# Optimization experiments

Hardware: AMD Instinct MI355X
Metric: run time of the kernel (lower is better)

The kernel has to match this reference:

```python
import jax, jax.numpy as jnp
import numpy as np

B, W, L = 32768, 5, 20            # batch, words per example, max chars per word
WV, CV = 50000, 100               # word vocab, char vocab
CE, OC, K = 32, 30, 3             # char embed dim, conv out channels (=window_size), kernel
WE, HID, TAGS = 50, 100, 36       # word embed dim, fc1 hidden, output tags


def setup_inputs() -> dict:
    key = jax.random.key(0)
    ks = jax.random.split(key, 8)
    inp = jax.random.randint(ks[0], (B, W, 1 + L), 0, 100, dtype=jnp.int32)
    embedding_matrix = jax.random.normal(ks[1], (WV, WE), jnp.float32).at[0].set(0.0)  # padding_idx=0, frozen
    char_emb = jax.random.normal(ks[2], (CV, CE), jnp.float32).at[0].set(0.0)          # padding_idx=0
    conv_w = jax.random.normal(ks[3], (OC, CE, K), jnp.float32) * 0.1
    conv_b = jnp.zeros((OC,), jnp.float32)
    fc1_w = jax.random.normal(ks[4], (HID, (WE + OC) * W), jnp.float32) * 0.05
    fc1_b = jnp.zeros((HID,), jnp.float32)
    out_w = jax.random.normal(ks[5], (TAGS, HID), jnp.float32) * 0.1
    out_b = jnp.zeros((TAGS,), jnp.float32)
    return dict(input=inp, embedding_matrix=embedding_matrix, char_emb=char_emb,
                conv_w=conv_w, conv_b=conv_b, fc1_w=fc1_w, fc1_b=fc1_b,
                out_w=out_w, out_b=out_b)


def reference(input, embedding_matrix, char_emb, conv_w, conv_b, fc1_w, fc1_b, out_w, out_b):
    b = input.shape[0]
    word_ids = input[:, :, 0]                 # [B, W]
    char_ids = input[:, :, 1:]                # [B, W, L]
    we = embedding_matrix[word_ids]           # [B, W, 50]
    ce = char_emb[char_ids]                   # [B, W, L, CE]
    # conv1d over char axis, batched over all B*W words at once
    x = ce.reshape(b * W, L, CE).transpose(0, 2, 1)        # [B*W, CE, L]
    conv = jax.lax.conv_general_dilated(
        x, conv_w, window_strides=(1,), padding='VALID',
        dimension_numbers=('NCH', 'OIH', 'NCH')) + conv_b[None, :, None]  # [B*W, OC, L-2]
    pooled = conv.max(axis=2).reshape(b, W, OC)            # max pool over time
    feats = jnp.concatenate([we, pooled], axis=-1).reshape(b, -1)  # [B, (50+OC)*W]
    h = jnp.tanh(feats @ fc1_w.T + fc1_b)     # dropout is a no-op at inference
    return h @ out_w.T + out_b                # [B, 36]
```

## Files before the change

### kernel.cpp

```cpp
#include <hip/hip_runtime.h>

#define B_TOT 32768
#define OC 30
#define HID 100
#define TAGS 36

#define WS_TH  0
#define WS_FC1 6000
#define WS_OUT 29296
#define WS_F   40960

typedef __attribute__((ext_vector_type(8))) _Float16 half8;
typedef __attribute__((ext_vector_type(2))) _Float16 h2v;
typedef __attribute__((ext_vector_type(4))) float f32x4;

__device__ inline half8 ash8(uint4 u) {
    union { uint4 a; half8 b; } v; v.a = u; return v.b;
}
__device__ inline unsigned int h2u(h2v h) {
    union { h2v a; unsigned int b; } v; v.a = h; return v.b;
}
__device__ inline h2v u2h(unsigned int u) {
    union { unsigned int a; h2v b; } v; v.a = u; return v.b;
}
__device__ inline unsigned int pk_f16(float a, float b) {
    h2v h; h.x = (_Float16)a; h.y = (_Float16)b; return h2u(h);
}

__global__ void prep(const float* __restrict__ conv_w,
                     const float* __restrict__ char_emb,
                     const float* __restrict__ fc1_w,
                     const float* __restrict__ out_w,
                     unsigned int* __restrict__ ws) {
    int idx = blockIdx.x * 256 + threadIdx.x;
    if (idx < 6000) {
        int rd = idx % 20, row = idx / 20;
        int c = row % 100, k = row / 100;
        float v[2];
        #pragma unroll
        for (int e = 0; e < 2; ++e) {
            int oc = rd * 2 + e;
            float s = 0.f;
            if (oc < OC) {
                for (int ce = 0; ce < 32; ++ce)
                    s += char_emb[c * 32 + ce] * conv_w[(oc * 32 + ce) * 3 + k];
            }
            v[e] = s;
        }
        ws[WS_TH + idx] = pk_f16(v[0], v[1]);
    } else if (idx < 6000 + 23296) {
        int t = idx - 6000;
        int dw = t & 3, lane = (t >> 2) & 63, chunk = t >> 8;
        int ks = chunk % 13, nt = chunk / 13;
        int j = nt * 16 + (lane & 15);
        int k = ks * 32 + (lane >> 4) * 8 + dw * 2;
        float a = (j < HID && k     < 400) ? fc1_w[j * 400 + k]     : 0.f;
        float b = (j < HID && k + 1 < 400) ? fc1_w[j * 400 + k + 1] : 0.f;
        ws[WS_FC1 + t] = pk_f16(a, b);
    } else if (idx < 29296 + 3072) {
        int t = idx - 29296;
        int dw = t & 3, lane = (t >> 2) & 63, chunk = t >> 8;
        int ks = chunk % 4, nt = chunk / 4;
        int j = nt * 16 + (lane & 15);
        int k = ks * 32 + (lane >> 4) * 8 + dw * 2;
        float a = (j < TAGS && k     < HID) ? out_w[j * 100 + k]     : 0.f;
        float b = (j < TAGS && k + 1 < HID) ? out_w[j * 100 + k + 1] : 0.f;
        ws[WS_OUT + t] = pk_f16(a, b);
    }
}

__global__ __launch_bounds__(256)
void feat(const int*   __restrict__ input,
          const float* __restrict__ emb,
          const float* __restrict__ conv_b,
          unsigned int* __restrict__ ws)
{
    __shared__ unsigned int Ths[6000];

    const int tid   = threadIdx.x;
    const int item0 = blockIdx.x * 16;
    unsigned int* Fg = ws + WS_F;

    for (int idx = tid; idx < 6000; idx += 256) Ths[idx] = ws[WS_TH + idx];
    __syncthreads();

    if (tid < 128) Fg[(item0 + (tid >> 3)) * 208 + 200 + (tid & 7)] = 0;

    for (int idx = tid; idx < 2000; idx += 256) {
        int ph = idx % 25;
        int w  = (idx / 25) % 5;
        int i  = idx / 125;
        int wid = input[(item0 + i) * 105 + w * 21];
        float2 e = *(const float2*)&emb[wid * 50 + ph * 2];
        Fg[(item0 + i) * 208 + w * 40 + ph] = pk_f16(e.x, e.y);
    }

    {
        const int q4  = tid & 3;
        const int oc0 = q4 * 8;
        h2v bias[4];
        #pragma unroll
        for (int d = 0; d < 4; ++d) {
            int a = oc0 + 2 * d, b = a + 1;
            bias[d].x = (_Float16)(a < OC ? conv_b[a] : 0.f);
            bias[d].y = (_Float16)(b < OC ? conv_b[b] : 0.f);
        }
        for (int task = tid >> 2; task < 80; task += 64) {
            int i = task / 5, w = task % 5;
            const int* cp = &input[(item0 + i) * 105 + w * 21 + 1];
            int c[20];
            #pragma unroll
            for (int p = 0; p < 20; ++p) c[p] = cp[p];
            h2v m[4];
            #pragma unroll
            for (int d = 0; d < 4; ++d) { m[d].x = (_Float16)(-30000.f); m[d].y = (_Float16)(-30000.f); }
            #pragma unroll 6
            for (int p = 0; p < 18; ++p) {
                uint4 ra = *(const uint4*)&Ths[c[p    ] * 20        + q4 * 4];
                uint4 rb = *(const uint4*)&Ths[c[p + 1] * 20 + 2000 + q4 * 4];
                uint4 rc = *(const uint4*)&Ths[c[p + 2] * 20 + 4000 + q4 * 4];
                unsigned int* pa = (unsigned int*)&ra;
                unsigned int* pb = (unsigned int*)&rb;
                unsigned int* pc = (unsigned int*)&rc;
                #pragma unroll
                for (int d = 0; d < 4; ++d) {
                    h2v s = u2h(pa[d]) + u2h(pb[d]) + u2h(pc[d]);
                    m[d] = __builtin_elementwise_max(m[d], s);
                }
            }
            int base = (item0 + i) * 208 + w * 40 + 25 + q4 * 4;
            Fg[base]     = h2u(m[0] + bias[0]);
            Fg[base + 1] = h2u(m[1] + bias[1]);
            Fg[base + 2] = h2u(m[2] + bias[2]);
            if (q4 < 3) Fg[base + 3] = h2u(m[3] + bias[3]);
        }
    }
}

__global__ __launch_bounds__(256)
void gemm(const float* __restrict__ fc1_b,
          const float* __restrict__ out_b,
          const unsigned int* __restrict__ ws,
          float*       __restrict__ out)
{
    __shared__ unsigned int Hh[4][16 * 68];

    const int tid  = threadIdx.x;
    const int wv   = tid >> 6;
    const int lane = tid & 63;
    const int ln15 = lane & 15;
    const int quad = lane >> 4;
    const int item0 = blockIdx.x * 64 + wv * 16;
    unsigned int* Hw = &Hh[wv][0];
    const unsigned int* Fg = ws + WS_F;

    f32x4 acc[7];
    #pragma unroll
    for (int t = 0; t < 7; ++t) acc[t] = f32x4{0, 0, 0, 0};
    {
        const uint4* wp = (const uint4*)(ws + WS_FC1);
        const unsigned int* arow = Fg + (item0 + ln15) * 208 + quad * 4;
        for (int ks = 0; ks < 13; ++ks) {
            half8 a = ash8(*(const uint4*)(arow + ks * 16));
            #pragma unroll
            for (int t = 0; t < 7; ++t) {
                uint4 bv = wp[(t * 13 + ks) * 64 + lane];
                acc[t] = __builtin_amdgcn_mfma_f32_16x16x32_f16(a, ash8(bv), acc[t], 0, 0, 0);
            }
        }
    }

    {
        for (int t2 = lane; t2 < 224; t2 += 64) {
            int i = t2 / 14, d = t2 % 14;
            Hw[i * 68 + 50 + d] = 0;
        }
        unsigned short* Hs = (unsigned short*)Hw;
        #pragma unroll
        for (int t = 0; t < 7; ++t) {
            int j = t * 16 + ln15;
            if (j < HID) {
                float bj = fc1_b[j];
                #pragma unroll
                for (int r = 0; r < 4; ++r) {
                    int it = quad * 4 + r;
                    float hv = tanhf(acc[t][r] + bj);
                    _Float16 h = (_Float16)hv;
                    Hs[it * 136 + j] = *reinterpret_cast<unsigned short*>(&h);
                }
            }
        }
    }

    {
        f32x4 oacc[3];
        #pragma unroll
        for (int t = 0; t < 3; ++t) oacc[t] = f32x4{0, 0, 0, 0};
        const uint4* wpo = (const uint4*)(ws + WS_OUT);
        const int aoff = ln15 * 68 + quad * 4;
        #pragma unroll
        for (int ks = 0; ks < 4; ++ks) {
            half8 a = ash8(*(const uint4*)&Hw[aoff + ks * 16]);
            #pragma unroll
            for (int t = 0; t < 3; ++t) {
                uint4 bv = wpo[(t * 4 + ks) * 64 + lane];
                oacc[t] = __builtin_amdgcn_mfma_f32_16x16x32_f16(a, ash8(bv), oacc[t], 0, 0, 0);
            }
        }
        #pragma unroll
        for (int t = 0; t < 3; ++t) {
            int o = t * 16 + ln15;
            if (o < TAGS) {
                float bo = out_b[o];
                #pragma unroll
                for (int r = 0; r < 4; ++r) {
                    int it = item0 + quad * 4 + r;
                    out[it * TAGS + o] = oacc[t][r] + bo;
                }
            }
        }
    }
}

extern "C" void kernel_launch(void* const* d_in, const int* in_sizes, int n_in,
                              void* d_out, int out_size, void* d_ws, size_t ws_size,
                              hipStream_t stream) {
    const int*   input  = (const int*)  d_in[0];
    const float* emb    = (const float*)d_in[1];
    const float* char_e = (const float*)d_in[2];
    const float* conv_w = (const float*)d_in[3];
    const float* conv_b = (const float*)d_in[4];
    const float* fc1_w  = (const float*)d_in[5];
    const float* fc1_b  = (const float*)d_in[6];
    const float* out_w  = (const float*)d_in[7];
    const float* out_b  = (const float*)d_in[8];
    unsigned int* ws = (unsigned int*)d_ws;

    prep<<<127, 256, 0, stream>>>(conv_w, char_e, fc1_w, out_w, ws);
    feat<<<B_TOT / 16, 256, 0, stream>>>(input, emb, conv_b, ws);
    gemm<<<B_TOT / 64, 256, 0, stream>>>(fc1_b, out_b, ws, (float*)d_out);
}
```

Measured before the change: 127.5 us.

## Fuse feature extraction and MLP into one kernel with LDS-resident features

Merges the feat and gemm kernels so each wave builds its 16 items' feature rows in shared memory and runs the fc1/out MFMA GEMMs directly from LDS. This removes the global round trip of the fp16 feature buffer and one kernel launch. It also relays out the conv lookup table so each quarter-lane group reads a contiguous slice, and replaces tanhf with an exp/rcp approximation. In exchange, each block loads the 24KB table for 64 items instead of 16, which repeats the table fill fewer times, and LDS use per block grows to about 78KB, limiting occupancy.

Measured after the change: 114.1 us. 10.5% less time.

```diff
diff --git a/kernel.cpp b/kernel.cpp
--- a/kernel.cpp
+++ b/kernel.cpp
@@ -8,7 +8,6 @@
 #define WS_TH  0
 #define WS_FC1 6000
 #define WS_OUT 29296
-#define WS_F   40960
 
 typedef __attribute__((ext_vector_type(8))) _Float16 half8;
 typedef __attribute__((ext_vector_type(2))) _Float16 h2v;
@@ -25,6 +24,12 @@
 }
 __device__ inline unsigned int pk_f16(float a, float b) {
     h2v h; h.x = (_Float16)a; h.y = (_Float16)b; return h2u(h);
+}
+__device__ inline float fast_tanh(float x) {
+    float ax = __builtin_fabsf(x);
+    float e  = __expf(2.0f * ax);
+    float r  = 1.0f - 2.0f * __builtin_amdgcn_rcpf(e + 1.0f);
+    return __builtin_copysignf(r, x);
 }
 
 __global__ void prep(const float* __restrict__ conv_w,
@@ -34,8 +39,12 @@
                      unsigned int* __restrict__ ws) {
     int idx = blockIdx.x * 256 + threadIdx.x;
     if (idx < 6000) {
-        int rd = idx % 20, row = idx / 20;
-        int c = row % 100, k = row / 100;
+        int d  = idx & 3;
+        int t  = idx >> 2;
+        int c  = t % 100;
+        int kg = t / 100;
+        int g  = kg % 5, k = kg / 5;
+        int rd = g * 4 + d;
         float v[2];
         #pragma unroll
         for (int e = 0; e < 2; ++e) {
@@ -69,34 +78,51 @@
     }
 }
 
-__global__ __launch_bounds__(256)
-void feat(const int*   __restrict__ input,
-          const float* __restrict__ emb,
-          const float* __restrict__ conv_b,
-          unsigned int* __restrict__ ws)
+__global__ __launch_bounds__(256, 2)
+void fused(const int*   __restrict__ input,
+           const float* __restrict__ emb,
+           const float* __restrict__ conv_b,
+           const float* __restrict__ fc1_b,
+           const float* __restrict__ out_b,
+           const unsigned int* __restrict__ ws,
+           float*       __restrict__ out)
 {
-    __shared__ unsigned int Ths[6000];
-
-    const int tid   = threadIdx.x;
-    const int item0 = blockIdx.x * 16;
-    unsigned int* Fg = ws + WS_F;
-
-    for (int idx = tid; idx < 6000; idx += 256) Ths[idx] = ws[WS_TH + idx];
+    __shared__ __align__(16) unsigned int Ths[6000];
+    __shared__ __align__(16) unsigned int FL[64 * 212];
+
+    const int tid  = threadIdx.x;
+    const int wv   = tid >> 6;
+    const int lane = tid & 63;
+    const int ln15 = lane & 15;
+    const int quad = lane >> 4;
+    const int gi0  = blockIdx.x * 64 + wv * 16;
+    unsigned int* Fw = &FL[wv * (16 * 212)];
+
+    {
+        const uint4* src = (const uint4*)(ws + WS_TH);
+        uint4* dst = (uint4*)Ths;
+        for (int idx = tid; idx < 1500; idx += 256) dst[idx] = src[idx];
+    }
     __syncthreads();
 
-    if (tid < 128) Fg[(item0 + (tid >> 3)) * 208 + 200 + (tid & 7)] = 0;
-
-    for (int idx = tid; idx < 2000; idx += 256) {
+    #pragma unroll
+    for (int r = 0; r < 2; ++r) {
+        int idx = lane + r * 64;
+        Fw[(idx >> 3) * 212 + 200 + (idx & 7)] = 0;
+    }
+
+    #pragma unroll 4
+    for (int idx = lane; idx < 2000; idx += 64) {
         int ph = idx % 25;
         int w  = (idx / 25) % 5;
         int i  = idx / 125;
-        int wid = input[(item0 + i) * 105 + w * 21];
+        int wid = input[(gi0 + i) * 105 + w * 21];
         float2 e = *(const float2*)&emb[wid * 50 + ph * 2];
-        Fg[(item0 + i) * 208 + w * 40 + ph] = pk_f16(e.x, e.y);
-    }
-
-    {
-        const int q4  = tid & 3;
+        Fw[i * 212 + w * 40 + ph] = pk_f16(e.x, e.y);
+    }
+
+    {
+        const int q4  = lane & 3;
         const int oc0 = q4 * 8;
         h2v bias[4];
         #pragma unroll
@@ -105,9 +131,14 @@
             bias[d].x = (_Float16)(a < OC ? conv_b[a] : 0.f);
             bias[d].y = (_Float16)(b < OC ? conv_b[b] : 0.f);
         }
-        for (int task = tid >> 2; task < 80; task += 64) {
+        const unsigned int* T0 = &Ths[q4 * 400];
+        const unsigned int* T1 = &Ths[q4 * 400 + 2000];
+        const unsigned int* T2 = &Ths[q4 * 400 + 4000];
+        #pragma unroll
+        for (int it = 0; it < 5; ++it) {
+            int task = (lane >> 2) + it * 16;
             int i = task / 5, w = task % 5;
-            const int* cp = &input[(item0 + i) * 105 + w * 21 + 1];
+            const int* cp = &input[(gi0 + i) * 105 + w * 21 + 1];
             int c[20];
             #pragma unroll
             for (int p = 0; p < 20; ++p) c[p] = cp[p];
@@ -116,9 +147,9 @@
             for (int d = 0; d < 4; ++d) { m[d].x = (_Float16)(-30000.f); m[d].y = (_Float16)(-30000.f); }
             #pragma unroll 6
             for (int p = 0; p < 18; ++p) {
-                uint4 ra = *(const uint4*)&Ths[c[p    ] * 20        + q4 * 4];
-                uint4 rb = *(const uint4*)&Ths[c[p + 1] * 20 + 2000 + q4 * 4];
-                uint4 rc = *(const uint4*)&Ths[c[p + 2] * 20 + 4000 + q4 * 4];
+                uint4 ra = *(const uint4*)&T0[c[p    ] * 4];
+                uint4 rb = *(const uint4*)&T1[c[p + 1] * 4];
+                uint4 rc = *(const uint4*)&T2[c[p + 2] * 4];
                 unsigned int* pa = (unsigned int*)&ra;
                 unsigned int* pb = (unsigned int*)&rb;
                 unsigned int* pc = (unsigned int*)&rc;
@@ -128,40 +159,26 @@
                     m[d] = __builtin_elementwise_max(m[d], s);
                 }
             }
-            int base = (item0 + i) * 208 + w * 40 + 25 + q4 * 4;
-            Fg[base]     = h2u(m[0] + bias[0]);
-            Fg[base + 1] = h2u(m[1] + bias[1]);
-            Fg[base + 2] = h2u(m[2] + bias[2]);
-            if (q4 < 3) Fg[base + 3] = h2u(m[3] + bias[3]);
-        }
-    }
-}
-
-__global__ __launch_bounds__(256)
-void gemm(const float* __restrict__ fc1_b,
-          const float* __restrict__ out_b,
-          const unsigned int* __restrict__ ws,
-          float*       __restrict__ out)
-{
-    __shared__ unsigned int Hh[4][16 * 68];
-
-    const int tid  = threadIdx.x;
-    const int wv   = tid >> 6;
-    const int lane = tid & 63;
-    const int ln15 = lane & 15;
-    const int quad = lane >> 4;
-    const int item0 = blockIdx.x * 64 + wv * 16;
-    unsigned int* Hw = &Hh[wv][0];
-    const unsigned int* Fg = ws + WS_F;
+            int base = i * 212 + w * 40 + 25 + q4 * 4;
+            Fw[base]     = h2u(m[0] + bias[0]);
+            Fw[base + 1] = h2u(m[1] + bias[1]);
+            Fw[base + 2] = h2u(m[2] + bias[2]);
+            if (q4 < 3) Fw[base + 3] = h2u(m[3] + bias[3]);
+        }
+    }
 
     f32x4 acc[7];
     #pragma unroll
     for (int t = 0; t < 7; ++t) acc[t] = f32x4{0, 0, 0, 0};
     {
         const uint4* wp = (const uint4*)(ws + WS_FC1);
-        const unsigned int* arow = Fg + (item0 + ln15) * 208 + quad * 4;
+        const unsigned int* arow = &Fw[ln15 * 212 + quad * 4];
+        uint4 af[13];
+        #pragma unroll
+        for (int ks = 0; ks < 13; ++ks) af[ks] = *(const uint4*)(arow + ks * 16);
+        #pragma unroll
         for (int ks = 0; ks < 13; ++ks) {
-            half8 a = ash8(*(const uint4*)(arow + ks * 16));
+            half8 a = ash8(af[ks]);
             #pragma unroll
             for (int t = 0; t < 7; ++t) {
                 uint4 bv = wp[(t * 13 + ks) * 64 + lane];
@@ -170,6 +187,7 @@
         }
     }
 
+    unsigned int* Hw = Fw;
     {
         for (int t2 = lane; t2 < 224; t2 += 64) {
             int i = t2 / 14, d = t2 % 14;
@@ -184,7 +202,7 @@
                 #pragma unroll
                 for (int r = 0; r < 4; ++r) {
                     int it = quad * 4 + r;
-                    float hv = tanhf(acc[t][r] + bj);
+                    float hv = fast_tanh(acc[t][r] + bj);
                     _Float16 h = (_Float16)hv;
                     Hs[it * 136 + j] = *reinterpret_cast<unsigned short*>(&h);
                 }
@@ -214,7 +232,7 @@
                 float bo = out_b[o];
                 #pragma unroll
                 for (int r = 0; r < 4; ++r) {
-                    int it = item0 + quad * 4 + r;
+                    int it = gi0 + quad * 4 + r;
                     out[it * TAGS + o] = oacc[t][r] + bo;
                 }
             }
@@ -237,6 +255,5 @@
     unsigned int* ws = (unsigned int*)d_ws;
 
     prep<<<127, 256, 0, stream>>>(conv_w, char_e, fc1_w, out_w, ws);
-    feat<<<B_TOT / 16, 256, 0, stream>>>(input, emb, conv_b, ws);
-    gemm<<<B_TOT / 64, 256, 0, stream>>>(fc1_b, out_b, ws, (float*)d_out);
-}
+    fused<<<B_TOT / 64, 256, 0, stream>>>(input, emb, conv_b, fc1_b, out_b, ws, (float*)d_out);
+}
```
